# Performance work log

Hardware: AMD Instinct MI355X
Metric: run time of the kernel (lower is better)

Reference implementation:

```python
import jax, jax.numpy as jnp
import numpy as np

D_MODEL, D_K, D_V, H = 1024, 64, 64, 16
B, NQ, NK = 4, 1024, 1024
HID = D_MODEL // 2


def _dwg(x, W1, b1, W2, b2):
    # DynamicWeightGenerator: sigmoid(fc2(relu(fc1(x))))
    h = jax.nn.relu(jnp.einsum('bnd,hd->bnh', x, W1) + b1)
    return jax.nn.sigmoid(jnp.einsum('bnh,dh->bnd', h, W2) + b2)


def setup_inputs() -> dict:
    key = jax.random.key(0)
    ks = jax.random.split(key, 32)
    s = 0.02
    inp = {
        'queries': jax.random.normal(ks[0], (B, NQ, D_MODEL), jnp.float32),
        'keys': jax.random.normal(ks[1], (B, NK, D_MODEL), jnp.float32),
        'values': jax.random.normal(ks[2], (B, NK, D_MODEL), jnp.float32),
        'attention_mask': jax.random.randint(ks[3], (B, 1, NQ, NK), 0, 2) > 0,
        'attention_weights': jax.random.uniform(ks[4], (B, H, NQ, NK), jnp.float32),
        'memory': jax.random.normal(ks[5], (B, NK), jnp.float32),
        # projections (torch Linear convention: y = x @ W.T + b)
        'Wq': jax.random.normal(ks[6], (H * D_K, D_MODEL), jnp.float32) * s,
        'bq': jnp.zeros((H * D_K,), jnp.float32),
        'Wk': jax.random.normal(ks[7], (H * D_K, D_MODEL), jnp.float32) * s,
        'bk': jnp.zeros((H * D_K,), jnp.float32),
        'Wv': jax.random.normal(ks[8], (H * D_V, D_MODEL), jnp.float32) * s,
        'bv': jnp.zeros((H * D_V,), jnp.float32),
        'Wo': jax.random.normal(ks[9], (D_MODEL, H * D_V), jnp.float32) * s,
        'bo': jnp.zeros((D_MODEL,), jnp.float32),
        'Wmm': jax.random.normal(ks[10], (H * D_V, 1), jnp.float32) * s,
        'bmm': jnp.zeros((H * D_V,), jnp.float32),
    }
    for i, tag in enumerate(['q', 'k', 'v']):
        k0, k1 = ks[11 + 2 * i], ks[12 + 2 * i]
        inp[f'W1{tag}'] = jax.random.normal(k0, (HID, D_MODEL), jnp.float32) * s
        inp[f'b1{tag}'] = jnp.zeros((HID,), jnp.float32)
        inp[f'W2{tag}'] = jax.random.normal(k1, (D_MODEL, HID), jnp.float32) * s
        inp[f'b2{tag}'] = jnp.zeros((D_MODEL,), jnp.float32)
    return inp


def reference(queries, keys, values, attention_mask, attention_weights, memory,
              Wq, bq, Wk, bk, Wv, bv, Wo, bo, Wmm, bmm,
              W1q, b1q, W2q, b2q, W1k, b1k, W2k, b2k, W1v, b1v, W2v, b2v):
    b_s, nq = queries.shape[:2]
    nk = keys.shape[1]
    # dynamic elementwise gating of inputs
    q_in = queries * _dwg(queries, W1q, b1q, W2q, b2q)
    k_in = keys * _dwg(keys, W1k, b1k, W2k, b2k)
    v_in = values * _dwg(values, W1v, b1v, W2v, b2v)
    # projections -> (b, h, n, d)
    q = (jnp.einsum('bnd,ed->bne', q_in, Wq) + bq).reshape(b_s, nq, H, D_K).transpose(0, 2, 1, 3)
    k = (jnp.einsum('bnd,ed->bne', k_in, Wk) + bk).reshape(b_s, nk, H, D_K).transpose(0, 2, 1, 3)
    v = (jnp.einsum('bnd,ed->bne', v_in, Wv) + bv).reshape(b_s, nk, H, D_V).transpose(0, 2, 1, 3)
    # per-token memory factor: fc_mm(memory[..., None]) -> (b, h, nk, d_k)
    mm = (memory[..., None] * Wmm[:, 0] + bmm).reshape(b_s, nk, H, D_K).transpose(0, 2, 1, 3)
    att = jnp.einsum('bhqd,bhkd->bhqk', q, k * mm) / np.sqrt(D_K).astype(np.float32)
    att = att * attention_weights                         # custom scaling (slice [:nk] == full)
    att = jnp.where(attention_mask, -jnp.inf, att)        # masked_fill
    att = jax.nn.softmax(att, axis=-1)
    out = jnp.einsum('bhqk,bhkd->bhqd', att, v * mm)      # (b, h, nq, d_v)
    out = out.transpose(0, 2, 1, 3).reshape(b_s, nq, H * D_V)
    return jnp.einsum('bne,de->bnd', out, Wo) + bo
```

## Files before the change

kernel.cpp:

```cpp
#include <hip/hip_runtime.h>
#include <hip/hip_bf16.h>

#define BB    4
#define NN    1024
#define DM    1024
#define HH    16
#define HID   512
#define TT    (BB * NN)

typedef __attribute__((ext_vector_type(8))) short bf16x8;
typedef __attribute__((ext_vector_type(4))) float f32x4;

__device__ __forceinline__ ushort f2bfu(float f) {
    __hip_bfloat16 h = __float2bfloat16(f);
    return __builtin_bit_cast(ushort, h);
}

__device__ __forceinline__ f32x4 mfma16(bf16x8 a, bf16x8 b, f32x4 c) {
    return __builtin_amdgcn_mfma_f32_16x16x32_bf16(a, b, c, 0, 0, 0);
}

__device__ __forceinline__ void gll16(const void* g, void* l) {
    __builtin_amdgcn_global_load_lds(
        (const __attribute__((address_space(1))) unsigned int*)g,
        (__attribute__((address_space(3))) unsigned int*)l, 16, 0, 0);
}

__global__ void detect_mask_kernel(const unsigned char* __restrict__ m,
                                   int nbytes, int* __restrict__ flags) {
    int stride = blockDim.x * gridDim.x;
    int hi = 0, lo = 0;
    for (int i = blockIdx.x * blockDim.x + threadIdx.x; i < nbytes; i += stride) {
        unsigned char v = m[i];
        if (v) { if (i & 3) hi = 1; else lo = 1; }
    }
    if (hi) atomicOr(&flags[0], 1);
    if (lo) atomicOr(&flags[1], 1);
}

template <int NS>
struct CvtArgs { const float* s[NS]; ushort* d[NS]; };

template <int NS>
__global__ __launch_bounds__(256) void cvt_multi(CvtArgs<NS> a, int n4) {
    int total = n4 * NS;
    int stride = blockDim.x * gridDim.x;
    for (int i = blockIdx.x * blockDim.x + threadIdx.x; i < total; i += stride) {
        const float* sp = a.s[0];
        ushort* dp = a.d[0];
        #pragma unroll
        for (int k = 1; k < NS; ++k) {
            bool ge = i >= k * n4;
            sp = ge ? a.s[k] : sp;
            dp = ge ? a.d[k] : dp;
        }
        int j = i % n4;
        float4 v = ((const float4*)sp)[j];
        uint2 o;
        o.x = (unsigned)f2bfu(v.x) | ((unsigned)f2bfu(v.y) << 16);
        o.y = (unsigned)f2bfu(v.z) | ((unsigned)f2bfu(v.w) << 16);
        ((uint2*)dp)[j] = o;
    }
}

struct GB {
    const ushort* A[3]; const ushort* W[3];
    const float* bias[3]; void* C[3]; const float* X[3];
};

template <int EP>
__global__ __launch_bounds__(256) void gemm_bf16(
    GB gb, int M, int N, int K,
    const float* __restrict__ mem, const float* __restrict__ Wmm,
    const float* __restrict__ bmm)
{
    __shared__ __align__(16) ushort As[128 * 64];
    __shared__ __align__(16) ushort Bs[128 * 64];
    const int z = blockIdx.z;
    const ushort* A = gb.A[z];
    const ushort* W = gb.W[z];
    const float* bias = gb.bias[z];
    void* Cout = gb.C[z];
    const float* X = gb.X[z];

    const int tid = threadIdx.x;
    const int lane = tid & 63, w = tid >> 6;
    const int lc = lane & 15, lg = lane >> 4;
    const int m0 = blockIdx.x * 128, n0 = blockIdx.y * 128;
    const int wm = (w >> 1) * 64, wn = (w & 1) * 64;
    const int srow = lane >> 3, scol = 8 * ((lane & 7) ^ srow);
    const int swl = (lc & 7) << 3;

    f32x4 acc[4][4];
    #pragma unroll
    for (int i = 0; i < 4; ++i)
        #pragma unroll
        for (int j = 0; j < 4; ++j)
            acc[i][j] = (f32x4){0.f, 0.f, 0.f, 0.f};

    #pragma unroll
    for (int ci = 0; ci < 4; ++ci) {
        int c = w + ci * 4;
        gll16(&A[(size_t)(m0 + c * 8 + srow) * K + 0 + scol], &As[c * 512]);
        gll16(&W[(size_t)(n0 + c * 8 + srow) * K + 0 + scol], &Bs[c * 512]);
    }

    for (int k0 = 0; k0 < K; k0 += 64) {
        __syncthreads();
        bf16x8 af[4][2], bfr[4][2];
        #pragma unroll
        for (int mi = 0; mi < 4; ++mi) {
            int row = wm + mi * 16 + lc;
            af[mi][0] = *(const bf16x8*)&As[row * 64 + ((lg * 8) ^ swl)];
            af[mi][1] = *(const bf16x8*)&As[row * 64 + ((32 + lg * 8) ^ swl)];
        }
        #pragma unroll
        for (int nj = 0; nj < 4; ++nj) {
            int row = wn + nj * 16 + lc;
            bfr[nj][0] = *(const bf16x8*)&Bs[row * 64 + ((lg * 8) ^ swl)];
            bfr[nj][1] = *(const bf16x8*)&Bs[row * 64 + ((32 + lg * 8) ^ swl)];
        }
        #pragma unroll
        for (int mi = 0; mi < 4; ++mi)
            #pragma unroll
            for (int nj = 0; nj < 4; ++nj) {
                acc[mi][nj] = mfma16(af[mi][0], bfr[nj][0], acc[mi][nj]);
                acc[mi][nj] = mfma16(af[mi][1], bfr[nj][1], acc[mi][nj]);
            }
        __syncthreads();
        if (k0 + 64 < K) {
            int kn = k0 + 64;
            #pragma unroll
            for (int ci = 0; ci < 4; ++ci) {
                int c = w + ci * 4;
                gll16(&A[(size_t)(m0 + c * 8 + srow) * K + kn + scol], &As[c * 512]);
                gll16(&W[(size_t)(n0 + c * 8 + srow) * K + kn + scol], &Bs[c * 512]);
            }
        }
    }

    #pragma unroll
    for (int nj = 0; nj < 4; ++nj) {
        int e = n0 + wn + nj * 16 + lc;
        float bv = bias[e];
        float wmv = 0.f, bmv = 0.f;
        if (EP == 7) { wmv = Wmm[e]; bmv = bmm[e]; }
        #pragma unroll
        for (int mi = 0; mi < 4; ++mi) {
            int mbase = m0 + wm + mi * 16 + lg * 4;
            if (EP == 7 && z == 2) {
                ushort u[4];
                #pragma unroll
                for (int r = 0; r < 4; ++r) {
                    float v = (acc[mi][nj][r] + bv) * (mem[mbase + r] * wmv + bmv);
                    u[r] = f2bfu(v);
                }
                int bb = mbase >> 10, n = mbase & 1023;
                size_t off = ((size_t)(bb * HH + (e >> 6)) * 64 + (e & 63)) * NN + n;
                uint2 pk;
                pk.x = (unsigned)u[0] | ((unsigned)u[1] << 16);
                pk.y = (unsigned)u[2] | ((unsigned)u[3] << 16);
                *(uint2*)&((ushort*)Cout)[off] = pk;
            } else {
                #pragma unroll
                for (int r = 0; r < 4; ++r) {
                    int m = mbase + r;
                    float v = acc[mi][nj][r] + bv;
                    if (EP == 1) v = fmaxf(v, 0.f);
                    if (EP == 2) v = X[(size_t)m * N + e] * (1.f / (1.f + __expf(-v)));
                    if (EP == 7) {
                        if (z == 0) v = v * 0.125f;
                        else        v = v * (mem[m] * wmv + bmv);
                    }
                    size_t off = (size_t)m * N + e;
                    if (EP == 4) ((float*)Cout)[off] = v;
                    else         ((ushort*)Cout)[off] = f2bfu(v);
                }
            }
        }
    }
}

__global__ __launch_bounds__(256) void attn_mfma(
    const ushort* __restrict__ qp, const ushort* __restrict__ kp,
    const ushort* __restrict__ vt, const float* __restrict__ aw,
    const void* __restrict__ maskp, const int* __restrict__ mflags,
    ushort* __restrict__ ob)
{
    __shared__ __align__(16) ushort Qs[64 * 64];
    __shared__ __align__(16) ushort Ks[64 * 64];
    __shared__ __align__(16) ushort Vs[64 * 64];
    __shared__ __align__(16) ushort Ps[64 * 64];
    const int tid = threadIdx.x, lane = tid & 63, w = tid >> 6;
    const int lc = lane & 15, lg = lane >> 4;
    const int qt = blockIdx.x, bh = blockIdx.y;
    const int b = bh >> 4, h = bh & 15;
    const int q0 = qt * 64, wq = w * 16;
    const int mode = mflags[0] ? (mflags[1] ? 1 : 2) : 0;
    const int srow = lane >> 3, scol = 8 * ((lane & 7) ^ srow);
    const int swl = (lc & 7) << 3;

    #pragma unroll
    for (int ci = 0; ci < 2; ++ci) {
        int c = w + ci * 4;
        gll16(&qp[(size_t)(b * NN + q0 + c * 8 + srow) * DM + h * 64 + scol], &Qs[c * 512]);
        gll16(&kp[(size_t)(b * NN + 0 + c * 8 + srow) * DM + h * 64 + scol], &Ks[c * 512]);
        gll16(&vt[(size_t)(bh * 64 + c * 8 + srow) * NN + 0 + scol], &Vs[c * 512]);
    }

    f32x4 oacc[4];
    #pragma unroll
    for (int i = 0; i < 4; ++i) oacc[i] = (f32x4){0.f, 0.f, 0.f, 0.f};
    float psum = 0.f;
    const int q = q0 + wq + lc;
    const float* awrow = aw + ((size_t)(bh) * NN + q) * NN;
    const size_t mrowo = ((size_t)b * NN + q) * NN;

    for (int t = 0; t < 16; ++t) {
        const int k0 = t * 64;
        __syncthreads();

        bf16x8 bq0 = *(const bf16x8*)&Qs[(wq + lc) * 64 + ((lg * 8) ^ swl)];
        bf16x8 bq1 = *(const bf16x8*)&Qs[(wq + lc) * 64 + ((32 + lg * 8) ^ swl)];
        f32x4 sacc[4];
        #pragma unroll
        for (int mi = 0; mi < 4; ++mi) {
            int krow = mi * 16 + lc;
            bf16x8 a0 = *(const bf16x8*)&Ks[krow * 64 + ((lg * 8) ^ swl)];
            bf16x8 a1 = *(const bf16x8*)&Ks[krow * 64 + ((32 + lg * 8) ^ swl)];
            f32x4 s = (f32x4){0.f, 0.f, 0.f, 0.f};
            s = mfma16(a0, bq0, s);
            s = mfma16(a1, bq1, s);
            sacc[mi] = s;
        }

        #pragma unroll
        for (int mi = 0; mi < 4; ++mi) {
            int kb = k0 + mi * 16 + lg * 4;
            float4 awv = *(const float4*)&awrow[kb];
            float pv[4];
            unsigned mk[4];
            if (mode == 0) {
                int4 mv = *(const int4*)&((const int*)maskp)[mrowo + kb];
                mk[0] = mv.x != 0; mk[1] = mv.y != 0; mk[2] = mv.z != 0; mk[3] = mv.w != 0;
            } else if (mode == 1) {
                unsigned mu = *(const unsigned*)&((const unsigned char*)maskp)[mrowo + kb];
                mk[0] = mu & 0xffu; mk[1] = (mu >> 8) & 0xffu;
                mk[2] = (mu >> 16) & 0xffu; mk[3] = (mu >> 24) & 0xffu;
            } else {
                float4 mv = *(const float4*)&((const float*)maskp)[mrowo + kb];
                mk[0] = mv.x != 0.f; mk[1] = mv.y != 0.f; mk[2] = mv.z != 0.f; mk[3] = mv.w != 0.f;
            }
            const float aww[4] = {awv.x, awv.y, awv.z, awv.w};
            #pragma unroll
            for (int r = 0; r < 4; ++r) {
                float sv = sacc[mi][r] * aww[r];
                pv[r] = mk[r] ? 0.f : __expf(sv);
                psum += pv[r];
            }
            uint2 pk;
            pk.x = (unsigned)f2bfu(pv[0]) | ((unsigned)f2bfu(pv[1]) << 16);
            pk.y = (unsigned)f2bfu(pv[2]) | ((unsigned)f2bfu(pv[3]) << 16);
            *(uint2*)&Ps[(wq + lc) * 64 + ((mi * 16 + lg * 4) ^ swl)] = pk;
        }

        #pragma unroll
        for (int kk = 0; kk < 2; ++kk) {
            bf16x8 pa = *(const bf16x8*)&Ps[(wq + lc) * 64 + ((kk * 32 + lg * 8) ^ swl)];
            #pragma unroll
            for (int nj = 0; nj < 4; ++nj) {
                bf16x8 vb = *(const bf16x8*)&Vs[(nj * 16 + lc) * 64 + ((kk * 32 + lg * 8) ^ swl)];
                oacc[nj] = mfma16(pa, vb, oacc[nj]);
            }
        }
        __syncthreads();
        if (t < 15) {
            int kn = k0 + 64;
            #pragma unroll
            for (int ci = 0; ci < 2; ++ci) {
                int c = w + ci * 4;
                gll16(&kp[(size_t)(b * NN + kn + c * 8 + srow) * DM + h * 64 + scol], &Ks[c * 512]);
                gll16(&vt[(size_t)(bh * 64 + c * 8 + srow) * NN + kn + scol], &Vs[c * 512]);
            }
        }
    }

    psum += __shfl_xor(psum, 16);
    psum += __shfl_xor(psum, 32);
    float inv = 1.0f / psum;
    float invr[4];
    #pragma unroll
    for (int r = 0; r < 4; ++r)
        invr[r] = __shfl(inv, (lane & 48) | (lg * 4 + r));

    #pragma unroll
    for (int nj = 0; nj < 4; ++nj)
        #pragma unroll
        for (int r = 0; r < 4; ++r) {
            int qq = q0 + wq + lg * 4 + r;
            float v = oacc[nj][r] * invr[r];
            ob[(size_t)(b * NN + qq) * DM + h * 64 + nj * 16 + lc] = f2bfu(v);
        }
}

extern "C" void kernel_launch(void* const* d_in, const int* in_sizes, int n_in,
                              void* d_out, int out_size, void* d_ws, size_t ws_size,
                              hipStream_t stream) {
    const float* xin_f[3] = {(const float*)d_in[0], (const float*)d_in[1], (const float*)d_in[2]};
    const void*  maskp   = d_in[3];
    const float* aw      = (const float*)d_in[4];
    const float* memv    = (const float*)d_in[5];
    const float* Wp_f[3] = {(const float*)d_in[6], (const float*)d_in[8], (const float*)d_in[10]};
    const float* bp[3]   = {(const float*)d_in[7], (const float*)d_in[9], (const float*)d_in[11]};
    const float* Wo_f  = (const float*)d_in[12];  const float* bo  = (const float*)d_in[13];
    const float* Wmm = (const float*)d_in[14];    const float* bmm = (const float*)d_in[15];
    const float* W1f[3] = {(const float*)d_in[16], (const float*)d_in[20], (const float*)d_in[24]};
    const float* b1a[3] = {(const float*)d_in[17], (const float*)d_in[21], (const float*)d_in[25]};
    const float* W2f[3] = {(const float*)d_in[18], (const float*)d_in[22], (const float*)d_in[26]};
    const float* b2a[3] = {(const float*)d_in[19], (const float*)d_in[23], (const float*)d_in[27]};

    char* p = (char*)d_ws;
    auto alloc = [&](size_t bytes) { char* r = p; p += (bytes + 255) & ~(size_t)255; return r; };
    int*    mflags = (int*)alloc(256);
    ushort* xbf[3]; for (int t = 0; t < 3; ++t) xbf[t] = (ushort*)alloc((size_t)TT * DM * 2);
    ushort* Wpb[3]; for (int t = 0; t < 3; ++t) Wpb[t] = (ushort*)alloc((size_t)DM * DM * 2);
    ushort* Wob  = (ushort*)alloc((size_t)DM * DM * 2);
    ushort* W1b[3]; for (int t = 0; t < 3; ++t) W1b[t] = (ushort*)alloc((size_t)HID * DM * 2);
    ushort* W2b[3]; for (int t = 0; t < 3; ++t) W2b[t] = (ushort*)alloc((size_t)DM * HID * 2);
    ushort* hbuf[3]; for (int t = 0; t < 3; ++t) hbuf[t] = (ushort*)alloc((size_t)TT * HID * 2);
    ushort* xg[3];  for (int t = 0; t < 3; ++t) xg[t] = (ushort*)alloc((size_t)TT * DM * 2);
    ushort* qpb  = (ushort*)alloc((size_t)TT * DM * 2);
    ushort* ksb  = (ushort*)alloc((size_t)TT * DM * 2);
    ushort* vtb  = (ushort*)alloc((size_t)TT * DM * 2);
    ushort* obuf = (ushort*)alloc((size_t)TT * DM * 2);

    hipMemsetAsync(mflags, 0, 8, stream);
    detect_mask_kernel<<<512, 256, 0, stream>>>((const unsigned char*)maskp,
                                                BB * NN * NN, mflags);

    {
        CvtArgs<3> a;
        for (int t = 0; t < 3; ++t) { a.s[t] = xin_f[t]; a.d[t] = xbf[t]; }
        cvt_multi<3><<<2048, 256, 0, stream>>>(a, TT * DM / 4);
    }
    {
        CvtArgs<4> a;
        a.s[0] = Wp_f[0]; a.d[0] = Wpb[0];
        a.s[1] = Wp_f[1]; a.d[1] = Wpb[1];
        a.s[2] = Wp_f[2]; a.d[2] = Wpb[2];
        a.s[3] = Wo_f;    a.d[3] = Wob;
        cvt_multi<4><<<2048, 256, 0, stream>>>(a, DM * DM / 4);
    }
    {
        CvtArgs<6> a;
        for (int t = 0; t < 3; ++t) { a.s[t] = W1f[t]; a.d[t] = W1b[t]; }
        for (int t = 0; t < 3; ++t) { a.s[3 + t] = W2f[t]; a.d[3 + t] = W2b[t]; }
        cvt_multi<6><<<2048, 256, 0, stream>>>(a, HID * DM / 4);
    }

    const dim3 blk(256);
    GB g1 = {}, g2 = {}, g3 = {}, g4 = {};
    for (int t = 0; t < 3; ++t) {
        g1.A[t] = xbf[t];  g1.W[t] = W1b[t]; g1.bias[t] = b1a[t]; g1.C[t] = hbuf[t];
        g2.A[t] = hbuf[t]; g2.W[t] = W2b[t]; g2.bias[t] = b2a[t]; g2.C[t] = xg[t]; g2.X[t] = xin_f[t];
        g3.A[t] = xg[t];   g3.W[t] = Wpb[t]; g3.bias[t] = bp[t];
    }
    g3.C[0] = qpb; g3.C[1] = ksb; g3.C[2] = vtb;
    g4.A[0] = obuf; g4.W[0] = Wob; g4.bias[0] = bo; g4.C[0] = d_out;

    gemm_bf16<1><<<dim3(TT / 128, HID / 128, 3), blk, 0, stream>>>(g1, TT, HID, DM, nullptr, nullptr, nullptr);
    gemm_bf16<2><<<dim3(TT / 128, DM / 128, 3), blk, 0, stream>>>(g2, TT, DM, HID, nullptr, nullptr, nullptr);
    gemm_bf16<7><<<dim3(TT / 128, DM / 128, 3), blk, 0, stream>>>(g3, TT, DM, DM, memv, Wmm, bmm);

    attn_mfma<<<dim3(NN / 64, BB * HH), blk, 0, stream>>>(qpb, ksb, vtb, aw,
                                                          maskp, mflags, obuf);

    gemm_bf16<4><<<dim3(TT / 128, DM / 128, 1), blk, 0, stream>>>(g4, TT, DM, DM, nullptr, nullptr, nullptr);
}
```

Before: 302.7 us.

## Double-buffer K/V tiles in attention, prefetch mask/weights, read gate input as bf16

After: 316.3 us. 1.04x slower.

```diff
diff --git a/kernel.cpp b/kernel.cpp
--- a/kernel.cpp
+++ b/kernel.cpp
@@ -14,6 +14,11 @@
 __device__ __forceinline__ ushort f2bfu(float f) {
     __hip_bfloat16 h = __float2bfloat16(f);
     return __builtin_bit_cast(ushort, h);
+}
+
+__device__ __forceinline__ float bfu2f(ushort u) {
+    __hip_bfloat16 h = __builtin_bit_cast(__hip_bfloat16, u);
+    return __bfloat162float(h);
 }
 
 __device__ __forceinline__ f32x4 mfma16(bf16x8 a, bf16x8 b, f32x4 c) {
@@ -65,7 +70,7 @@
 
 struct GB {
     const ushort* A[3]; const ushort* W[3];
-    const float* bias[3]; void* C[3]; const float* X[3];
+    const float* bias[3]; void* C[3]; const ushort* X[3];
 };
 
 template <int EP>
@@ -81,7 +86,7 @@
     const ushort* W = gb.W[z];
     const float* bias = gb.bias[z];
     void* Cout = gb.C[z];
-    const float* X = gb.X[z];
+    const ushort* X = gb.X[z];
 
     const int tid = threadIdx.x;
     const int lane = tid & 63, w = tid >> 6;
@@ -167,7 +172,7 @@
                     int m = mbase + r;
                     float v = acc[mi][nj][r] + bv;
                     if (EP == 1) v = fmaxf(v, 0.f);
-                    if (EP == 2) v = X[(size_t)m * N + e] * (1.f / (1.f + __expf(-v)));
+                    if (EP == 2) v = bfu2f(X[(size_t)m * N + e]) * (1.f / (1.f + __expf(-v)));
                     if (EP == 7) {
                         if (z == 0) v = v * 0.125f;
                         else        v = v * (mem[m] * wmv + bmv);
@@ -187,9 +192,8 @@
     const void* __restrict__ maskp, const int* __restrict__ mflags,
     ushort* __restrict__ ob)
 {
-    __shared__ __align__(16) ushort Qs[64 * 64];
-    __shared__ __align__(16) ushort Ks[64 * 64];
-    __shared__ __align__(16) ushort Vs[64 * 64];
+    __shared__ __align__(16) ushort Ks[2][64 * 64];
+    __shared__ __align__(16) ushort Vs[2][64 * 64];
     __shared__ __align__(16) ushort Ps[64 * 64];
     const int tid = threadIdx.x, lane = tid & 63, w = tid >> 6;
     const int lc = lane & 15, lg = lane >> 4;
@@ -200,34 +204,68 @@
     const int srow = lane >> 3, scol = 8 * ((lane & 7) ^ srow);
     const int swl = (lc & 7) << 3;
 
+    const ushort* qrow = &qp[(size_t)(b * NN + q0 + wq + lc) * DM + h * 64];
+    bf16x8 bq0 = *(const bf16x8*)&qrow[lg * 8];
+    bf16x8 bq1 = *(const bf16x8*)&qrow[32 + lg * 8];
+
     #pragma unroll
     for (int ci = 0; ci < 2; ++ci) {
         int c = w + ci * 4;
-        gll16(&qp[(size_t)(b * NN + q0 + c * 8 + srow) * DM + h * 64 + scol], &Qs[c * 512]);
-        gll16(&kp[(size_t)(b * NN + 0 + c * 8 + srow) * DM + h * 64 + scol], &Ks[c * 512]);
-        gll16(&vt[(size_t)(bh * 64 + c * 8 + srow) * NN + 0 + scol], &Vs[c * 512]);
-    }
+        gll16(&kp[(size_t)(b * NN + c * 8 + srow) * DM + h * 64 + scol], &Ks[0][c * 512]);
+        gll16(&vt[(size_t)(bh * 64 + c * 8 + srow) * NN + 0 + scol], &Vs[0][c * 512]);
+    }
+    __syncthreads();
 
     f32x4 oacc[4];
     #pragma unroll
     for (int i = 0; i < 4; ++i) oacc[i] = (f32x4){0.f, 0.f, 0.f, 0.f};
     float psum = 0.f;
     const int q = q0 + wq + lc;
-    const float* awrow = aw + ((size_t)(bh) * NN + q) * NN;
+    const float* awrow = aw + ((size_t)bh * NN + q) * NN;
     const size_t mrowo = ((size_t)b * NN + q) * NN;
 
     for (int t = 0; t < 16; ++t) {
         const int k0 = t * 64;
-        __syncthreads();
-
-        bf16x8 bq0 = *(const bf16x8*)&Qs[(wq + lc) * 64 + ((lg * 8) ^ swl)];
-        bf16x8 bq1 = *(const bf16x8*)&Qs[(wq + lc) * 64 + ((32 + lg * 8) ^ swl)];
+        const int cur = t & 1;
+        const ushort* Kc = Ks[cur];
+        const ushort* Vc = Vs[cur];
+
+        float4 awv[4];
+        #pragma unroll
+        for (int mi = 0; mi < 4; ++mi)
+            awv[mi] = *(const float4*)&awrow[k0 + mi * 16 + lg * 4];
+        int4 mvi[4]; unsigned mvb[4]; float4 mvf[4];
+        if (mode == 0) {
+            #pragma unroll
+            for (int mi = 0; mi < 4; ++mi)
+                mvi[mi] = *(const int4*)&((const int*)maskp)[mrowo + k0 + mi * 16 + lg * 4];
+        } else if (mode == 1) {
+            #pragma unroll
+            for (int mi = 0; mi < 4; ++mi)
+                mvb[mi] = *(const unsigned*)&((const unsigned char*)maskp)[mrowo + k0 + mi * 16 + lg * 4];
+        } else {
+            #pragma unroll
+            for (int mi = 0; mi < 4; ++mi)
+                mvf[mi] = *(const float4*)&((const float*)maskp)[mrowo + k0 + mi * 16 + lg * 4];
+        }
+        __builtin_amdgcn_sched_barrier(0);
+
+        if (t < 15) {
+            int kn = k0 + 64;
+            #pragma unroll
+            for (int ci = 0; ci < 2; ++ci) {
+                int c = w + ci * 4;
+                gll16(&kp[(size_t)(b * NN + kn + c * 8 + srow) * DM + h * 64 + scol], &Ks[cur ^ 1][c * 512]);
+                gll16(&vt[(size_t)(bh * 64 + c * 8 + srow) * NN + kn + scol], &Vs[cur ^ 1][c * 512]);
+            }
+        }
+
         f32x4 sacc[4];
         #pragma unroll
         for (int mi = 0; mi < 4; ++mi) {
             int krow = mi * 16 + lc;
-            bf16x8 a0 = *(const bf16x8*)&Ks[krow * 64 + ((lg * 8) ^ swl)];
-            bf16x8 a1 = *(const bf16x8*)&Ks[krow * 64 + ((32 + lg * 8) ^ swl)];
+            bf16x8 a0 = *(const bf16x8*)&Kc[krow * 64 + ((lg * 8) ^ swl)];
+            bf16x8 a1 = *(const bf16x8*)&Kc[krow * 64 + ((32 + lg * 8) ^ swl)];
             f32x4 s = (f32x4){0.f, 0.f, 0.f, 0.f};
             s = mfma16(a0, bq0, s);
             s = mfma16(a1, bq1, s);
@@ -236,22 +274,19 @@
 
         #pragma unroll
         for (int mi = 0; mi < 4; ++mi) {
-            int kb = k0 + mi * 16 + lg * 4;
-            float4 awv = *(const float4*)&awrow[kb];
-            float pv[4];
             unsigned mk[4];
             if (mode == 0) {
-                int4 mv = *(const int4*)&((const int*)maskp)[mrowo + kb];
-                mk[0] = mv.x != 0; mk[1] = mv.y != 0; mk[2] = mv.z != 0; mk[3] = mv.w != 0;
+                mk[0] = mvi[mi].x != 0; mk[1] = mvi[mi].y != 0;
+                mk[2] = mvi[mi].z != 0; mk[3] = mvi[mi].w != 0;
             } else if (mode == 1) {
-                unsigned mu = *(const unsigned*)&((const unsigned char*)maskp)[mrowo + kb];
-                mk[0] = mu & 0xffu; mk[1] = (mu >> 8) & 0xffu;
-                mk[2] = (mu >> 16) & 0xffu; mk[3] = (mu >> 24) & 0xffu;
+                mk[0] = mvb[mi] & 0xffu;        mk[1] = (mvb[mi] >> 8) & 0xffu;
+                mk[2] = (mvb[mi] >> 16) & 0xffu; mk[3] = (mvb[mi] >> 24) & 0xffu;
             } else {
-                float4 mv = *(const float4*)&((const float*)maskp)[mrowo + kb];
-                mk[0] = mv.x != 0.f; mk[1] = mv.y != 0.f; mk[2] = mv.z != 0.f; mk[3] = mv.w != 0.f;
-            }
-            const float aww[4] = {awv.x, awv.y, awv.z, awv.w};
+                mk[0] = mvf[mi].x != 0.f; mk[1] = mvf[mi].y != 0.f;
+                mk[2] = mvf[mi].z != 0.f; mk[3] = mvf[mi].w != 0.f;
+            }
+            const float aww[4] = {awv[mi].x, awv[mi].y, awv[mi].z, awv[mi].w};
+            float pv[4];
             #pragma unroll
             for (int r = 0; r < 4; ++r) {
                 float sv = sacc[mi][r] * aww[r];
@@ -269,20 +304,11 @@
             bf16x8 pa = *(const bf16x8*)&Ps[(wq + lc) * 64 + ((kk * 32 + lg * 8) ^ swl)];
             #pragma unroll
             for (int nj = 0; nj < 4; ++nj) {
-                bf16x8 vb = *(const bf16x8*)&Vs[(nj * 16 + lc) * 64 + ((kk * 32 + lg * 8) ^ swl)];
+                bf16x8 vb = *(const bf16x8*)&Vc[(nj * 16 + lc) * 64 + ((kk * 32 + lg * 8) ^ swl)];
                 oacc[nj] = mfma16(pa, vb, oacc[nj]);
             }
         }
         __syncthreads();
-        if (t < 15) {
-            int kn = k0 + 64;
-            #pragma unroll
-            for (int ci = 0; ci < 2; ++ci) {
-                int c = w + ci * 4;
-                gll16(&kp[(size_t)(b * NN + kn + c * 8 + srow) * DM + h * 64 + scol], &Ks[c * 512]);
-                gll16(&vt[(size_t)(bh * 64 + c * 8 + srow) * NN + kn + scol], &Vs[c * 512]);
-            }
-        }
     }
 
     psum += __shfl_xor(psum, 16);
@@ -362,7 +388,7 @@
     GB g1 = {}, g2 = {}, g3 = {}, g4 = {};
     for (int t = 0; t < 3; ++t) {
         g1.A[t] = xbf[t];  g1.W[t] = W1b[t]; g1.bias[t] = b1a[t]; g1.C[t] = hbuf[t];
-        g2.A[t] = hbuf[t]; g2.W[t] = W2b[t]; g2.bias[t] = b2a[t]; g2.C[t] = xg[t]; g2.X[t] = xin_f[t];
+        g2.A[t] = hbuf[t]; g2.W[t] = W2b[t]; g2.bias[t] = b2a[t]; g2.C[t] = xg[t]; g2.X[t] = xbf[t];
         g3.A[t] = xg[t];   g3.W[t] = Wpb[t]; g3.bias[t] = bp[t];
     }
     g3.C[0] = qpb; g3.C[1] = ksb; g3.C[2] = vtb;
```
